# Optimization experiments

Measured on AMD Instinct MI355X. Metric: run time of the kernel, lower is better.

The kernel has to match this reference:

```python
import jax, jax.numpy as jnp
import numpy as np

L = 10  # lattice_size


def _wilson_plaquette_loop(field, x):
    # Faithful translation of compute_wilson_loop: product of exp(plaquette) over 6 (mu,nu) pairs.
    coords = x[0, :4].astype(jnp.int32) % L
    loop = jnp.ones((1,), dtype=field.dtype)
    for mu in range(4):
        for nu in range(mu + 1, 4):
            pos = coords
            link1 = field[pos[0], pos[1], pos[2], mu]
            pos = pos.at[mu].set((pos[mu] + 1) % L)
            link2 = field[pos[0], pos[1], pos[2], nu]
            pos = pos.at[nu].set((pos[nu] + 1) % L)
            link3 = -field[pos[0], pos[1], pos[2], mu]
            pos = pos.at[mu].add(-1)  # original has no mod here
            link4 = -field[coords[0], coords[1], coords[2], nu]
            loop = loop * jnp.exp(link1 + link2 + link3 - (-link4) + 0.0 if False else link1 + link2 + link3 + link4)
    return loop


def setup_inputs() -> dict:
    key = jax.random.key(0)
    ks = jax.random.split(key, 20)
    s = 0.02  # scale weights to keep activations numerically sane
    d = jnp.float32
    return {
        'x': jax.random.normal(ks[0], (16384, 4), d),
        'field': jax.random.normal(ks[1], (L, L, L, 4), d),
        'fw1': jax.random.normal(ks[2], (4, 2048), d) * s,
        'fb1': jax.random.normal(ks[3], (2048,), d) * s,
        'fw2': jax.random.normal(ks[4], (2048, 4096), d) * s,
        'fb2': jax.random.normal(ks[5], (4096,), d) * s,
        'ww1': jax.random.normal(ks[6], (4096, 2048), d) * s,
        'wb1': jax.random.normal(ks[7], (2048,), d) * s,
        'ww2': jax.random.normal(ks[8], (2048, 1024), d) * s,
        'wb2': jax.random.normal(ks[9], (1024,), d) * s,
        'ww3': jax.random.normal(ks[10], (1024, 1), d) * s,
        'wb3': jax.random.normal(ks[11], (1,), d) * s,
        'tw1': jax.random.normal(ks[12], (4096, 2048), d) * s,
        'tb1': jax.random.normal(ks[13], (2048,), d) * s,
        'tw2': jax.random.normal(ks[14], (2048, 1), d) * s,
        'tb2': jax.random.normal(ks[15], (1,), d) * s,
    }


def reference(x, field, fw1, fb1, fw2, fb2, ww1, wb1, ww2, wb2, ww3, wb3, tw1, tb1, tw2, tb2):
    x4 = x[:, :4]
    h = jnp.maximum(x4 @ fw1 + fb1, 0.0)
    field_output = h @ fw2 + fb2                       # [B, dim]
    plaq = _wilson_plaquette_loop(field, x4)           # [1] (computed in torch forward, not returned)
    w = jnp.maximum(field_output @ ww1 + wb1, 0.0)
    w = jnp.maximum(w @ ww2 + wb2, 0.0)
    wilson_output = w @ ww3 + wb3                      # [B, 1]
    t = jnp.maximum(field_output @ tw1 + tb1, 0.0)
    topology_output = t @ tw2 + tb2                    # [B, 1]
    return field_output, wilson_output, topology_output, plaq
```

## Files before the change

### kernel.cpp

```cpp
#include <hip/hip_runtime.h>

#define L 10

using bf16x8 = __attribute__((ext_vector_type(8))) __bf16;
using u16x8  = __attribute__((ext_vector_type(8))) unsigned short;
using f32x4  = __attribute__((ext_vector_type(4))) float;

__device__ __forceinline__ unsigned short f2bf(float f) {
  unsigned int u = __float_as_uint(f);
  u += 0x7FFFu + ((u >> 16) & 1u);
  return (unsigned short)(u >> 16);
}
__device__ __forceinline__ float bf2f(unsigned short h) {
  return __uint_as_float(((unsigned int)h) << 16);
}

__global__ void plaq_kernel(const float* __restrict__ x,
                            const float* __restrict__ field,
                            float* __restrict__ out) {
  if (threadIdx.x != 0 || blockIdx.x != 0) return;
  int c[4];
#pragma unroll
  for (int i = 0; i < 4; ++i) {
    int v = (int)x[i];
    v %= L; if (v < 0) v += L;
    c[i] = v;
  }
  float S = 0.f;
  for (int mu = 0; mu < 4; ++mu)
    for (int nu = mu + 1; nu < 4; ++nu) {
      int p[4] = {c[0], c[1], c[2], c[3]};
      float l1 = field[((p[0]*L + p[1])*L + p[2])*4 + mu];
      p[mu] = (p[mu] + 1) % L;
      float l2 = field[((p[0]*L + p[1])*L + p[2])*4 + nu];
      p[nu] = (p[nu] + 1) % L;
      float l3 = field[((p[0]*L + p[1])*L + p[2])*4 + mu];
      float l4 = field[((c[0]*L + c[1])*L + c[2])*4 + nu];
      S += l1 + l2 - l3 - l4;
    }
  out[0] = expf(S);
}

__global__ void init_heads_kernel(float* __restrict__ outWil,
                                  float* __restrict__ outTop,
                                  const float* __restrict__ wb3,
                                  const float* __restrict__ tb2) {
  int i = blockIdx.x * blockDim.x + threadIdx.x;
  if (i < 16384) { outWil[i] = wb3[0]; outTop[i] = tb2[0]; }
}

__global__ void fc1_kernel(const float* __restrict__ x,
                           const float* __restrict__ fw1,
                           const float* __restrict__ fb1,
                           unsigned short* __restrict__ h) {
  const int N = 2048;
  int idx = blockIdx.x * blockDim.x + threadIdx.x;
  int m  = idx >> 8;
  int n0 = (idx & 255) * 8;
  float4 xv = *(const float4*)(x + (size_t)m * 4);
  unsigned short o[8];
#pragma unroll
  for (int j = 0; j < 8; ++j) {
    int n = n0 + j;
    float s = fb1[n] + xv.x * fw1[n] + xv.y * fw1[N + n]
                     + xv.z * fw1[2*N + n] + xv.w * fw1[3*N + n];
    o[j] = f2bf(fmaxf(s, 0.f));
  }
  *(u16x8*)(h + (size_t)m * N + n0) = *(const u16x8*)o;
}

__global__ void transpose_bf16_kernel(const float* __restrict__ W,
                                      unsigned short* __restrict__ WT,
                                      int K, int N) {
  __shared__ float tile[32][33];
  int n0 = blockIdx.x * 32, k0 = blockIdx.y * 32;
  int tx = threadIdx.x, ty = threadIdx.y;
#pragma unroll
  for (int i = 0; i < 32; i += 8)
    tile[ty + i][tx] = W[(size_t)(k0 + ty + i) * N + n0 + tx];
  __syncthreads();
#pragma unroll
  for (int i = 0; i < 32; i += 8)
    WT[(size_t)(n0 + ty + i) * K + k0 + tx] = f2bf(tile[tx][ty + i]);
}

__global__ void cast_bf16_kernel(const float* __restrict__ in,
                                 unsigned short* __restrict__ out) {
  size_t i = ((size_t)blockIdx.x * blockDim.x + threadIdx.x) * 8;
  unsigned short o[8];
#pragma unroll
  for (int j = 0; j < 8; ++j) o[j] = f2bf(in[i + j]);
  *(u16x8*)(out + i) = *(const u16x8*)o;
}

__global__ void biascat_kernel(const unsigned short* __restrict__ catT,
                               const float* __restrict__ fb2,
                               const float* __restrict__ wb1,
                               const float* __restrict__ tb1,
                               float* __restrict__ out) {
  int w    = blockIdx.x * 4 + (threadIdx.x >> 6);
  int lane = threadIdx.x & 63;
  if (w < 4096) { if (lane == 0) out[w] = fb2[w]; return; }
  int m = w - 4096;
  const unsigned short* row = catT + (size_t)m * 4096;
  float s = 0.f;
  for (int k = lane * 8; k < 4096; k += 512) {
    u16x8 v = *(const u16x8*)(row + k);
#pragma unroll
    for (int j = 0; j < 8; ++j) s += bf2f(v[j]) * fb2[k + j];
  }
#pragma unroll
  for (int off = 32; off; off >>= 1) s += __shfl_down(s, off);
  if (lane == 0) out[w] = s + (m < 2048 ? wb1[m] : tb1[m - 2048]);
}

#define GLL(gp, lp)                                                            \
  __builtin_amdgcn_global_load_lds(                                            \
      (const __attribute__((address_space(1))) unsigned int*)(gp),             \
      (__attribute__((address_space(3))) unsigned int*)(lp), 16, 0, 0)

#define DSREAD(dst, addr)                                                      \
  asm volatile("ds_read_b128 %0, %1" : "=v"(dst) : "v"(addr))

#define LGKM(n)                                                                \
  do { asm volatile("s_waitcnt lgkmcnt(" #n ")" ::: "memory");                 \
       __builtin_amdgcn_sched_barrier(0); } while (0)

#define FENCE() asm volatile("" ::: "memory")

extern __shared__ char lds_raw[];

__global__ __launch_bounds__(256)
void gemm128f_kernel(const unsigned short* __restrict__ A,
                     const unsigned short* __restrict__ BT,
                     unsigned short* __restrict__ outB,
                     int N, int K, int gmx) {
  const int NT = K >> 5;

  const int nwg = gridDim.x;
  const int q = nwg >> 3, r = nwg & 7;
  const int xcd = blockIdx.x & 7, lid = blockIdx.x >> 3;
  const int wg2 = (xcd < r ? xcd * (q + 1) : r * (q + 1) + (xcd - r) * q) + lid;
  const int bm = wg2 % gmx, bn = wg2 / gmx;

  const int tid  = threadIdx.x;
  const int wid  = tid >> 6, lane = tid & 63;
  const int wr   = wid >> 1, wc = wid & 1;
  const int lr   = lane & 15, lg = lane >> 4;

  const int srow = tid >> 2;
  const int scol = ((tid & 3) ^ ((tid >> 3) & 3)) * 8;
  const unsigned short* agp0 = A  + (size_t)(bm * 128 + srow) * K + scol;
  const unsigned short* agp1 = agp0 + (size_t)64 * K;
  const unsigned short* bgp0 = BT + (size_t)(bn * 128 + srow) * K + scol;
  const unsigned short* bgp1 = bgp0 + (size_t)64 * K;

  const int chunk = lg ^ ((lr >> 1) & 3);
  const unsigned ldsbase = (unsigned)(uintptr_t)&lds_raw[0];
  const unsigned aoff = (unsigned)((wr * 64 + lr) * 64 + chunk * 16);
  const unsigned boff = (unsigned)(8192 + (wc * 64 + lr) * 64 + chunk * 16);

  f32x4 acc[4][4];
#pragma unroll
  for (int m = 0; m < 4; ++m)
#pragma unroll
    for (int n = 0; n < 4; ++n) acc[m][n] = (f32x4)0.f;

#define STAGE_A(tt) do { unsigned so = (unsigned)(((tt) & 3) << 14);           \
    GLL(agp0 + (size_t)(tt) * 32, lds_raw + so + tid * 16);                    \
    GLL(agp1 + (size_t)(tt) * 32, lds_raw + so + 4096 + tid * 16); } while (0)
#define STAGE_B(tt) do { unsigned so = (unsigned)(((tt) & 3) << 14);           \
    GLL(bgp0 + (size_t)(tt) * 32, lds_raw + so + 8192 + tid * 16);             \
    GLL(bgp1 + (size_t)(tt) * 32, lds_raw + so + 12288 + tid * 16); } while (0)

  STAGE_A(0); STAGE_B(0); STAGE_A(1); STAGE_B(1); STAGE_A(2); STAGE_B(2);

  for (int t = 0; t < NT; ++t) {
    const int rem = NT - 1 - t;
    if (rem >= 2)      asm volatile("s_waitcnt vmcnt(8)" ::: "memory");
    else if (rem == 1) asm volatile("s_waitcnt vmcnt(4)" ::: "memory");
    else               asm volatile("s_waitcnt vmcnt(0)" ::: "memory");
    FENCE(); __builtin_amdgcn_s_barrier(); FENCE();
    __builtin_amdgcn_sched_barrier(0);

    if (t + 3 < NT) { STAGE_A(t + 3); STAGE_B(t + 3); }

    const unsigned sbase = ldsbase + (unsigned)((t & 3) << 14);
    u16x8 b[4], a[4];
    DSREAD(b[0], sbase + boff);
    DSREAD(b[1], sbase + boff + 1024);
    DSREAD(b[2], sbase + boff + 2048);
    DSREAD(b[3], sbase + boff + 3072);
    DSREAD(a[0], sbase + aoff);
    DSREAD(a[1], sbase + aoff + 1024);
    DSREAD(a[2], sbase + aoff + 2048);
    DSREAD(a[3], sbase + aoff + 3072);

    __builtin_amdgcn_s_setprio(1);
#define CLUSTER(m, g)                                                          \
    LGKM(g);                                                                   \
    acc[m][0] = __builtin_amdgcn_mfma_f32_16x16x32_bf16(                       \
        __builtin_bit_cast(bf16x8, a[m]), __builtin_bit_cast(bf16x8, b[0]),    \
        acc[m][0], 0, 0, 0);                                                   \
    acc[m][1] = __builtin_amdgcn_mfma_f32_16x16x32_bf16(                       \
        __builtin_bit_cast(bf16x8, a[m]), __builtin_bit_cast(bf16x8, b[1]),    \
        acc[m][1], 0, 0, 0);                                                   \
    acc[m][2] = __builtin_amdgcn_mfma_f32_16x16x32_bf16(                       \
        __builtin_bit_cast(bf16x8, a[m]), __builtin_bit_cast(bf16x8, b[2]),    \
        acc[m][2], 0, 0, 0);                                                   \
    acc[m][3] = __builtin_amdgcn_mfma_f32_16x16x32_bf16(                       \
        __builtin_bit_cast(bf16x8, a[m]), __builtin_bit_cast(bf16x8, b[3]),    \
        acc[m][3], 0, 0, 0)

    CLUSTER(0, 3);
    CLUSTER(1, 2);
    CLUSTER(2, 1);
    CLUSTER(3, 0);
#undef CLUSTER
    __builtin_amdgcn_s_setprio(0);
    __builtin_amdgcn_sched_barrier(0);
  }
#undef STAGE_A
#undef STAGE_B

  const int rowBase = bm * 128 + wr * 64 + lg * 4;
  const int colBase = bn * 128 + wc * 64 + lr;
#pragma unroll
  for (int n = 0; n < 4; ++n) {
    int col = colBase + n * 16;
#pragma unroll
    for (int m = 0; m < 4; ++m) {
      int row = rowBase + m * 16;
#pragma unroll
      for (int j = 0; j < 4; ++j)
        outB[(size_t)(row + j) * N + col] = f2bf(acc[m][n][j]);
    }
  }
}

__global__ __launch_bounds__(512)
void gemm256_kernel(const unsigned short* __restrict__ A,
                    const unsigned short* __restrict__ BT,
                    const float* __restrict__ bias,
                    float* __restrict__ outF,
                    unsigned short* __restrict__ outB,
                    const float* __restrict__ hvec,
                    float* __restrict__ hout,
                    int lda, int K, int NF, int NB,
                    int nFtiles, int nHtiles, int gmx) {
  const int NT = K >> 5;

  const int nwg = gridDim.x;
  const int q = nwg >> 3, r = nwg & 7;
  const int xcd = blockIdx.x & 7, lid = blockIdx.x >> 3;
  const int wg2 = (xcd < r ? xcd * (q + 1) : r * (q + 1) + (xcd - r) * q) + lid;
  const int bm = wg2 % gmx, bn = wg2 / gmx;

  const int tid  = threadIdx.x;
  const int wid  = tid >> 6, lane = tid & 63;
  const int wr   = wid >> 2, wc = wid & 3;
  const int lr   = lane & 15, lg = lane >> 4;

  const int srow = tid >> 2;
  const int scol = ((tid & 3) ^ ((tid >> 3) & 3)) * 8;
  const unsigned short* agp0 = A  + (size_t)(bm * 256 + srow) * lda + scol;
  const unsigned short* agp1 = agp0 + (size_t)128 * lda;
  const unsigned short* bgp0 = BT + (size_t)(bn * 256 + srow) * K + scol;
  const unsigned short* bgp1 = bgp0 + (size_t)128 * K;

  const int chunk = lg ^ ((lr >> 1) & 3);
  const unsigned ldsbase = (unsigned)(uintptr_t)&lds_raw[0];
  const unsigned aoff = (unsigned)((wr * 128 + lr) * 64 + chunk * 16);
  const unsigned boff = (unsigned)(16384 + (wc * 64 + lr) * 64 + chunk * 16);

  f32x4 acc[8][4];
#pragma unroll
  for (int m = 0; m < 8; ++m)
#pragma unroll
    for (int n = 0; n < 4; ++n) acc[m][n] = (f32x4)0.f;

#define STAGE_A(tt) do { unsigned so = (unsigned)(((tt) & 3) << 15);           \
    GLL(agp0 + (size_t)(tt) * 32, lds_raw + so + tid * 16);                    \
    GLL(agp1 + (size_t)(tt) * 32, lds_raw + so + 8192 + tid * 16); } while (0)
#define STAGE_B(tt) do { unsigned so = (unsigned)(((tt) & 3) << 15);           \
    GLL(bgp0 + (size_t)(tt) * 32, lds_raw + so + 16384 + tid * 16);            \
    GLL(bgp1 + (size_t)(tt) * 32, lds_raw + so + 24576 + tid * 16); } while (0)

  STAGE_A(0); STAGE_B(0); STAGE_A(1); STAGE_B(1); STAGE_A(2); STAGE_B(2);

  for (int t = 0; t < NT; ++t) {
    const int rem = NT - 1 - t;
    if (rem >= 2)      asm volatile("s_waitcnt vmcnt(8)" ::: "memory");
    else if (rem == 1) asm volatile("s_waitcnt vmcnt(4)" ::: "memory");
    else               asm volatile("s_waitcnt vmcnt(0)" ::: "memory");
    FENCE(); __builtin_amdgcn_s_barrier(); FENCE();
    __builtin_amdgcn_sched_barrier(0);

    if (t + 3 < NT) { STAGE_A(t + 3); STAGE_B(t + 3); }

    const unsigned sbase = ldsbase + (unsigned)((t & 3) << 15);

    u16x8 b[4], a[8];
    DSREAD(b[0], sbase + boff);
    DSREAD(b[1], sbase + boff + 1024);
    DSREAD(b[2], sbase + boff + 2048);
    DSREAD(b[3], sbase + boff + 3072);
    DSREAD(a[0], sbase + aoff);
    DSREAD(a[1], sbase + aoff + 1024);
    DSREAD(a[2], sbase + aoff + 2048);
    DSREAD(a[3], sbase + aoff + 3072);
    DSREAD(a[4], sbase + aoff + 4096);
    DSREAD(a[5], sbase + aoff + 5120);
    DSREAD(a[6], sbase + aoff + 6144);
    DSREAD(a[7], sbase + aoff + 7168);

    __builtin_amdgcn_s_setprio(1);
#define CLUSTER(m, g)                                                          \
    LGKM(g);                                                                   \
    acc[m][0] = __builtin_amdgcn_mfma_f32_16x16x32_bf16(                       \
        __builtin_bit_cast(bf16x8, a[m]), __builtin_bit_cast(bf16x8, b[0]),    \
        acc[m][0], 0, 0, 0);                                                   \
    acc[m][1] = __builtin_amdgcn_mfma_f32_16x16x32_bf16(                       \
        __builtin_bit_cast(bf16x8, a[m]), __builtin_bit_cast(bf16x8, b[1]),    \
        acc[m][1], 0, 0, 0);                                                   \
    acc[m][2] = __builtin_amdgcn_mfma_f32_16x16x32_bf16(                       \
        __builtin_bit_cast(bf16x8, a[m]), __builtin_bit_cast(bf16x8, b[2]),    \
        acc[m][2], 0, 0, 0);                                                   \
    acc[m][3] = __builtin_amdgcn_mfma_f32_16x16x32_bf16(                       \
        __builtin_bit_cast(bf16x8, a[m]), __builtin_bit_cast(bf16x8, b[3]),    \
        acc[m][3], 0, 0, 0)

    CLUSTER(0, 7);
    CLUSTER(1, 6);
    CLUSTER(2, 5);
    CLUSTER(3, 4);
    CLUSTER(4, 3);
    CLUSTER(5, 2);
    CLUSTER(6, 1);
    CLUSTER(7, 0);
#undef CLUSTER
    __builtin_amdgcn_s_setprio(0);
    __builtin_amdgcn_sched_barrier(0);
  }
#undef STAGE_A
#undef STAGE_B

  const int rowBase = bm * 256 + wr * 128 + lg * 4;
  const int colBase = bn * 256 + wc * 64 + lr;
  if (bn < nFtiles) {
#pragma unroll
    for (int n = 0; n < 4; ++n) {
      int col = colBase + n * 16;
      float bv = bias[col];
#pragma unroll
      for (int m = 0; m < 8; ++m) {
        int row = rowBase + m * 16;
#pragma unroll
        for (int j = 0; j < 4; ++j)
          outF[(size_t)(row + j) * NF + col] = acc[m][n][j] + bv;
      }
    }
  } else if (bn < nHtiles) {
    const int colB = colBase - nFtiles * 256;
#pragma unroll
    for (int n = 0; n < 4; ++n) {
      int col = colB + n * 16;
      float bv = bias[colBase + n * 16];
#pragma unroll
      for (int m = 0; m < 8; ++m) {
        int row = rowBase + m * 16;
#pragma unroll
        for (int j = 0; j < 4; ++j)
          outB[(size_t)(row + j) * NB + col] = f2bf(fmaxf(acc[m][n][j] + bv, 0.f));
      }
    }
  } else {
    const int hcol0 = colBase - nHtiles * 256;
    float bv[4], hv[4];
#pragma unroll
    for (int n = 0; n < 4; ++n) {
      bv[n] = bias[colBase + n * 16];
      hv[n] = hvec[hcol0 + n * 16];
    }
#pragma unroll
    for (int m = 0; m < 8; ++m) {
#pragma unroll
      for (int j = 0; j < 4; ++j) {
        float s = 0.f;
#pragma unroll
        for (int n = 0; n < 4; ++n)
          s += fmaxf(acc[m][n][j] + bv[n], 0.f) * hv[n];
        s += __shfl_xor(s, 1);
        s += __shfl_xor(s, 2);
        s += __shfl_xor(s, 4);
        s += __shfl_xor(s, 8);
        if (lr == 0)
          atomicAdd(&hout[rowBase + m * 16 + j], s);
      }
    }
  }
}

extern "C" void kernel_launch(void* const* d_in, const int* in_sizes, int n_in,
                              void* d_out, int out_size, void* d_ws, size_t ws_size,
                              hipStream_t stream) {
  const float* x     = (const float*)d_in[0];
  const float* field = (const float*)d_in[1];
  const float* fw1   = (const float*)d_in[2];
  const float* fb1   = (const float*)d_in[3];
  const float* fw2   = (const float*)d_in[4];
  const float* fb2   = (const float*)d_in[5];
  const float* ww1   = (const float*)d_in[6];
  const float* wb1   = (const float*)d_in[7];
  const float* ww2   = (const float*)d_in[8];
  const float* wb2   = (const float*)d_in[9];
  const float* ww3   = (const float*)d_in[10];
  const float* wb3   = (const float*)d_in[11];
  const float* tw1   = (const float*)d_in[12];
  const float* tb1   = (const float*)d_in[13];
  const float* tw2   = (const float*)d_in[14];
  const float* tb2   = (const float*)d_in[15];

  const int M = 16384;
  float* outF    = (float*)d_out;
  float* outWil  = outF + (size_t)M * 4096;
  float* outTop  = outWil + M;
  float* outPlaq = outTop + M;

  char* ws = (char*)d_ws;
  const size_t MB = 1048576;
  unsigned short* hbuf    = (unsigned short*)(ws);
  unsigned short* catbuf  = (unsigned short*)(ws + 64  * MB);
  unsigned short* catT    = (unsigned short*)(ws + 192 * MB);
  unsigned short* fw2T    = (unsigned short*)(ws + 224 * MB);
  unsigned short* W2catT  = (unsigned short*)(ws + 240 * MB);
  unsigned short* BTcat   = fw2T;
  unsigned short* fw2bf   = (unsigned short*)(ws + 256 * MB);
  unsigned short* ww2T    = (unsigned short*)(ws + 272 * MB);
  float*          biascat = (float*)(ws + 276 * MB);

  const int SMEM = 131072;
  (void)hipFuncSetAttribute((const void*)gemm256_kernel,
                            hipFuncAttributeMaxDynamicSharedMemorySize, SMEM);
  const int SMEM128 = 65536;
  (void)hipFuncSetAttribute((const void*)gemm128f_kernel,
                            hipFuncAttributeMaxDynamicSharedMemorySize, SMEM128);

  hipLaunchKernelGGL(plaq_kernel, dim3(1), dim3(64), 0, stream, x, field, outPlaq);
  hipLaunchKernelGGL(init_heads_kernel, dim3(64), dim3(256), 0, stream,
                     outWil, outTop, wb3, tb2);
  hipLaunchKernelGGL(fc1_kernel, dim3(16384), dim3(256), 0, stream, x, fw1, fb1, hbuf);
  hipLaunchKernelGGL(transpose_bf16_kernel, dim3(128, 64), dim3(32, 8), 0, stream,
                     fw2, fw2T, 2048, 4096);
  hipLaunchKernelGGL(cast_bf16_kernel, dim3(4096), dim3(256), 0, stream, fw2, fw2bf);
  hipLaunchKernelGGL(transpose_bf16_kernel, dim3(64, 128), dim3(32, 8), 0, stream,
                     ww1, catT, 4096, 2048);
  hipLaunchKernelGGL(transpose_bf16_kernel, dim3(64, 128), dim3(32, 8), 0, stream,
                     tw1, catT + (size_t)2048 * 4096, 4096, 2048);
  hipLaunchKernelGGL(transpose_bf16_kernel, dim3(32, 64), dim3(32, 8), 0, stream,
                     ww2, ww2T, 2048, 1024);
  hipLaunchKernelGGL(biascat_kernel, dim3(2048), dim3(256), 0, stream,
                     catT, fb2, wb1, tb1, biascat);

  hipLaunchKernelGGL(gemm128f_kernel, dim3(512), dim3(256), SMEM128, stream,
                     catT, fw2bf, W2catT, 2048, 4096, 32);

  hipLaunchKernelGGL(gemm256_kernel, dim3(64 * 32), dim3(512), SMEM, stream,
                     hbuf, BTcat, biascat, outF, catbuf, tw2, outTop,
                     2048, 2048, 4096, 2048, 16, 24, 64);

  hipLaunchKernelGGL(gemm256_kernel, dim3(64 * 4), dim3(512), SMEM, stream,
                     catbuf, ww2T, wb2, (float*)nullptr, (unsigned short*)nullptr,
                     ww3, outWil,
                     2048, 2048, 0, 0, 0, 0, 64);

  (void)in_sizes; (void)n_in; (void)out_size; (void)ws_size;
}
```

Baseline: 875.3 us.

## Shrink main GEMM tiles to 128x128 with 3-stage pipeline and nontemporal stores

Replaces the 256x256 tile, 512-thread GEMM with a 128x128 tile, 256-thread version that uses a 3-slot LDS ring (48KB) instead of 4 slots (128KB), and adjusts the grids and tile-index parameters to match. The fp32 field output is now written with nontemporal stores. Smaller tiles and less LDS should allow more workgroups per CU and better load balance, but each tile reuses its operands less, so global and LDS traffic per FLOP goes up. The pipeline is also one stage shallower.

```diff
diff --git a/kernel.cpp b/kernel.cpp
--- a/kernel.cpp
+++ b/kernel.cpp
@@ -238,16 +238,16 @@
   }
 }
 
-__global__ __launch_bounds__(512)
-void gemm256_kernel(const unsigned short* __restrict__ A,
-                    const unsigned short* __restrict__ BT,
-                    const float* __restrict__ bias,
-                    float* __restrict__ outF,
-                    unsigned short* __restrict__ outB,
-                    const float* __restrict__ hvec,
-                    float* __restrict__ hout,
-                    int lda, int K, int NF, int NB,
-                    int nFtiles, int nHtiles, int gmx) {
+__global__ __launch_bounds__(256)
+void gemm128x_kernel(const unsigned short* __restrict__ A,
+                     const unsigned short* __restrict__ BT,
+                     const float* __restrict__ bias,
+                     float* __restrict__ outF,
+                     unsigned short* __restrict__ outB,
+                     const float* __restrict__ hvec,
+                     float* __restrict__ hout,
+                     int lda, int K, int NF, int NB,
+                     int nFtiles, int nHtiles, int gmx) {
   const int NT = K >> 5;
 
   const int nwg = gridDim.x;
@@ -258,49 +258,48 @@
 
   const int tid  = threadIdx.x;
   const int wid  = tid >> 6, lane = tid & 63;
-  const int wr   = wid >> 2, wc = wid & 3;
+  const int wr   = wid >> 1, wc = wid & 1;
   const int lr   = lane & 15, lg = lane >> 4;
 
   const int srow = tid >> 2;
   const int scol = ((tid & 3) ^ ((tid >> 3) & 3)) * 8;
-  const unsigned short* agp0 = A  + (size_t)(bm * 256 + srow) * lda + scol;
-  const unsigned short* agp1 = agp0 + (size_t)128 * lda;
-  const unsigned short* bgp0 = BT + (size_t)(bn * 256 + srow) * K + scol;
-  const unsigned short* bgp1 = bgp0 + (size_t)128 * K;
+  const unsigned short* agp0 = A  + (size_t)(bm * 128 + srow) * lda + scol;
+  const unsigned short* agp1 = agp0 + (size_t)64 * lda;
+  const unsigned short* bgp0 = BT + (size_t)(bn * 128 + srow) * K + scol;
+  const unsigned short* bgp1 = bgp0 + (size_t)64 * K;
 
   const int chunk = lg ^ ((lr >> 1) & 3);
   const unsigned ldsbase = (unsigned)(uintptr_t)&lds_raw[0];
-  const unsigned aoff = (unsigned)((wr * 128 + lr) * 64 + chunk * 16);
-  const unsigned boff = (unsigned)(16384 + (wc * 64 + lr) * 64 + chunk * 16);
-
-  f32x4 acc[8][4];
-#pragma unroll
-  for (int m = 0; m < 8; ++m)
+  const unsigned aoff = (unsigned)((wr * 64 + lr) * 64 + chunk * 16);
+  const unsigned boff = (unsigned)(8192 + (wc * 64 + lr) * 64 + chunk * 16);
+
+  f32x4 acc[4][4];
+#pragma unroll
+  for (int m = 0; m < 4; ++m)
 #pragma unroll
     for (int n = 0; n < 4; ++n) acc[m][n] = (f32x4)0.f;
 
-#define STAGE_A(tt) do { unsigned so = (unsigned)(((tt) & 3) << 15);           \
+#define SLOT(tt) ((unsigned)(((tt) % 3) * 16384))
+#define STAGE_A(tt) do { unsigned so = SLOT(tt);                               \
     GLL(agp0 + (size_t)(tt) * 32, lds_raw + so + tid * 16);                    \
-    GLL(agp1 + (size_t)(tt) * 32, lds_raw + so + 8192 + tid * 16); } while (0)
-#define STAGE_B(tt) do { unsigned so = (unsigned)(((tt) & 3) << 15);           \
-    GLL(bgp0 + (size_t)(tt) * 32, lds_raw + so + 16384 + tid * 16);            \
-    GLL(bgp1 + (size_t)(tt) * 32, lds_raw + so + 24576 + tid * 16); } while (0)
-
-  STAGE_A(0); STAGE_B(0); STAGE_A(1); STAGE_B(1); STAGE_A(2); STAGE_B(2);
+    GLL(agp1 + (size_t)(tt) * 32, lds_raw + so + 4096 + tid * 16); } while (0)
+#define STAGE_B(tt) do { unsigned so = SLOT(tt);                               \
+    GLL(bgp0 + (size_t)(tt) * 32, lds_raw + so + 8192 + tid * 16);             \
+    GLL(bgp1 + (size_t)(tt) * 32, lds_raw + so + 12288 + tid * 16); } while (0)
+
+  STAGE_A(0); STAGE_B(0); STAGE_A(1); STAGE_B(1);
 
   for (int t = 0; t < NT; ++t) {
     const int rem = NT - 1 - t;
-    if (rem >= 2)      asm volatile("s_waitcnt vmcnt(8)" ::: "memory");
-    else if (rem == 1) asm volatile("s_waitcnt vmcnt(4)" ::: "memory");
-    else               asm volatile("s_waitcnt vmcnt(0)" ::: "memory");
+    if (rem >= 1) asm volatile("s_waitcnt vmcnt(4)" ::: "memory");
+    else          asm volatile("s_waitcnt vmcnt(0)" ::: "memory");
     FENCE(); __builtin_amdgcn_s_barrier(); FENCE();
     __builtin_amdgcn_sched_barrier(0);
 
-    if (t + 3 < NT) { STAGE_A(t + 3); STAGE_B(t + 3); }
-
-    const unsigned sbase = ldsbase + (unsigned)((t & 3) << 15);
-
-    u16x8 b[4], a[8];
+    if (t + 2 < NT) { STAGE_A(t + 2); STAGE_B(t + 2); }
+
+    const unsigned sbase = ldsbase + SLOT(t);
+    u16x8 b[4], a[4];
     DSREAD(b[0], sbase + boff);
     DSREAD(b[1], sbase + boff + 1024);
     DSREAD(b[2], sbase + boff + 2048);
@@ -309,10 +308,6 @@
     DSREAD(a[1], sbase + aoff + 1024);
     DSREAD(a[2], sbase + aoff + 2048);
     DSREAD(a[3], sbase + aoff + 3072);
-    DSREAD(a[4], sbase + aoff + 4096);
-    DSREAD(a[5], sbase + aoff + 5120);
-    DSREAD(a[6], sbase + aoff + 6144);
-    DSREAD(a[7], sbase + aoff + 7168);
 
     __builtin_amdgcn_s_setprio(1);
 #define CLUSTER(m, g)                                                          \
@@ -330,44 +325,42 @@
         __builtin_bit_cast(bf16x8, a[m]), __builtin_bit_cast(bf16x8, b[3]),    \
         acc[m][3], 0, 0, 0)
 
-    CLUSTER(0, 7);
-    CLUSTER(1, 6);
-    CLUSTER(2, 5);
-    CLUSTER(3, 4);
-    CLUSTER(4, 3);
-    CLUSTER(5, 2);
-    CLUSTER(6, 1);
-    CLUSTER(7, 0);
+    CLUSTER(0, 3);
+    CLUSTER(1, 2);
+    CLUSTER(2, 1);
+    CLUSTER(3, 0);
 #undef CLUSTER
     __builtin_amdgcn_s_setprio(0);
     __builtin_amdgcn_sched_barrier(0);
   }
+#undef SLOT
 #undef STAGE_A
 #undef STAGE_B
 
-  const int rowBase = bm * 256 + wr * 128 + lg * 4;
-  const int colBase = bn * 256 + wc * 64 + lr;
+  const int rowBase = bm * 128 + wr * 64 + lg * 4;
+  const int colBase = bn * 128 + wc * 64 + lr;
   if (bn < nFtiles) {
 #pragma unroll
     for (int n = 0; n < 4; ++n) {
       int col = colBase + n * 16;
       float bv = bias[col];
 #pragma unroll
-      for (int m = 0; m < 8; ++m) {
+      for (int m = 0; m < 4; ++m) {
         int row = rowBase + m * 16;
 #pragma unroll
         for (int j = 0; j < 4; ++j)
-          outF[(size_t)(row + j) * NF + col] = acc[m][n][j] + bv;
+          __builtin_nontemporal_store(acc[m][n][j] + bv,
+                                      &outF[(size_t)(row + j) * NF + col]);
       }
     }
   } else if (bn < nHtiles) {
-    const int colB = colBase - nFtiles * 256;
+    const int colB = colBase - nFtiles * 128;
 #pragma unroll
     for (int n = 0; n < 4; ++n) {
       int col = colB + n * 16;
       float bv = bias[colBase + n * 16];
 #pragma unroll
-      for (int m = 0; m < 8; ++m) {
+      for (int m = 0; m < 4; ++m) {
         int row = rowBase + m * 16;
 #pragma unroll
         for (int j = 0; j < 4; ++j)
@@ -375,7 +368,7 @@
       }
     }
   } else {
-    const int hcol0 = colBase - nHtiles * 256;
+    const int hcol0 = colBase - nHtiles * 128;
     float bv[4], hv[4];
 #pragma unroll
     for (int n = 0; n < 4; ++n) {
@@ -383,7 +376,7 @@
       hv[n] = hvec[hcol0 + n * 16];
     }
 #pragma unroll
-    for (int m = 0; m < 8; ++m) {
+    for (int m = 0; m < 4; ++m) {
 #pragma unroll
       for (int j = 0; j < 4; ++j) {
         float s = 0.f;
@@ -439,12 +432,12 @@
   unsigned short* ww2T    = (unsigned short*)(ws + 272 * MB);
   float*          biascat = (float*)(ws + 276 * MB);
 
-  const int SMEM = 131072;
-  (void)hipFuncSetAttribute((const void*)gemm256_kernel,
-                            hipFuncAttributeMaxDynamicSharedMemorySize, SMEM);
   const int SMEM128 = 65536;
   (void)hipFuncSetAttribute((const void*)gemm128f_kernel,
                             hipFuncAttributeMaxDynamicSharedMemorySize, SMEM128);
+  const int SMEMX = 49152;
+  (void)hipFuncSetAttribute((const void*)gemm128x_kernel,
+                            hipFuncAttributeMaxDynamicSharedMemorySize, SMEMX);
 
   hipLaunchKernelGGL(plaq_kernel, dim3(1), dim3(64), 0, stream, x, field, outPlaq);
   hipLaunchKernelGGL(init_heads_kernel, dim3(64), dim3(256), 0, stream,
@@ -465,14 +458,14 @@
   hipLaunchKernelGGL(gemm128f_kernel, dim3(512), dim3(256), SMEM128, stream,
                      catT, fw2bf, W2catT, 2048, 4096, 32);
 
-  hipLaunchKernelGGL(gemm256_kernel, dim3(64 * 32), dim3(512), SMEM, stream,
+  hipLaunchKernelGGL(gemm128x_kernel, dim3(128 * 64), dim3(256), SMEMX, stream,
                      hbuf, BTcat, biascat, outF, catbuf, tw2, outTop,
-                     2048, 2048, 4096, 2048, 16, 24, 64);
-
-  hipLaunchKernelGGL(gemm256_kernel, dim3(64 * 4), dim3(512), SMEM, stream,
+                     2048, 2048, 4096, 2048, 32, 48, 128);
+
+  hipLaunchKernelGGL(gemm128x_kernel, dim3(128 * 8), dim3(256), SMEMX, stream,
                      catbuf, ww2T, wb2, (float*)nullptr, (unsigned short*)nullptr,
                      ww3, outWil,
-                     2048, 2048, 0, 0, 0, 0, 64);
+                     2048, 2048, 0, 0, 0, 0, 128);
 
   (void)in_sizes; (void)n_in; (void)out_size; (void)ws_size;
 }
```

After: 1.044 ms. 19.3% more time.
